# Kernel tuning notes

Measured on AMD Instinct MI355X. Metric: run time of the kernel, lower is better.

Reference implementation:

```python
import jax, jax.numpy as jnp
import numpy as np

DIM = 256
HID = DIM * 16

def setup_inputs() -> dict:
    key = jax.random.key(0)
    ks = jax.random.split(key, 6)
    B, L = 4, 2048
    x = jax.random.normal(ks[0], (B, L, DIM), dtype=jnp.float32)
    # nn.Linear(dim, hidden): weight [H, D], bias [H]
    WB = jax.random.normal(ks[1], (HID, DIM), dtype=jnp.float32) / np.sqrt(DIM)
    bB = jax.random.normal(ks[2], (HID,), dtype=jnp.float32) * 0.01
    # nn.Linear(hidden, dim): weight [D, H], bias [D]
    WC = jax.random.normal(ks[3], (DIM, HID), dtype=jnp.float32) / np.sqrt(HID)
    bC = jax.random.normal(ks[4], (DIM,), dtype=jnp.float32) * 0.01
    A = jax.random.normal(ks[5], (HID,), dtype=jnp.float32)
    return {"x": x, "WB": WB, "bB": bB, "WC": WC, "bC": bC, "A": A}

def reference(x, WB, bB, WC, bC, A):
    # b = B(x): [B, L, H]
    b = jnp.einsum('bld,hd->blh', x, WB) + bB
    a = jax.nn.sigmoid(A)  # [H], time-invariant decay
    # h_t = a * h_{t-1} + b_t  (h_0 from zero state) -> associative scan over L
    a_seq = jnp.broadcast_to(a, b.shape)
    def comb(c1, c2):
        a1, u1 = c1
        a2, u2 = c2
        return (a1 * a2, a2 * u1 + u2)
    _, h = jax.lax.associative_scan(comb, (a_seq, b), axis=1)  # [B, L, H]
    # C(h): [B, L, D]
    return jnp.einsum('blh,dh->bld', h, WC) + bC
```

## Files before the change

kernel.cpp:

```cpp
#include <hip/hip_runtime.h>
#include <hip/hip_bf16.h>

#define DIMSZ 256
#define HID 4096
#define BATCH 4
#define SEQ 2048
#define NCH 64
#define CLEN 32
#define SPLITK2 4
#define KCHUNK (HID / SPLITK2)
#define BM2 32

typedef __bf16 bf16_t;
typedef __bf16 bf16x4 __attribute__((ext_vector_type(4)));
typedef __bf16 bf16x8 __attribute__((ext_vector_type(8)));
typedef float  f32x4  __attribute__((ext_vector_type(4)));

__device__ __forceinline__ float sigmoidf_dev(float x) {
    return 1.0f / (1.0f + __expf(-x));
}

__device__ __forceinline__ bf16x8 cvt8(const float* p) {
    bf16x8 o;
    #pragma unroll
    for (int j = 0; j < 8; j++) o[j] = (bf16_t)p[j];
    return o;
}

__global__ void prep_kernel(const float* __restrict__ x,
                            const float* __restrict__ WB,
                            const float* __restrict__ WC,
                            bf16_t* __restrict__ xt,
                            bf16_t* __restrict__ WBt,
                            bf16_t* __restrict__ Wt) {
    int i = blockIdx.x * blockDim.x + threadIdx.x;
    if (i < 262144) {
        int lane = i & 63, m16 = (i >> 6) & 511, ks = i >> 15;
        int row = m16 * 16 + (lane & 15);
        int k   = ks * 32 + (lane >> 4) * 8;
        *(bf16x8*)&xt[(size_t)i * 8] = cvt8(&x[(size_t)row * DIMSZ + k]);
    } else if (i < 393216) {
        int j = i - 262144;
        int lane = j & 63, n16 = (j >> 6) & 255, ks = j >> 14;
        int row = n16 * 16 + (lane & 15);
        int k   = ks * 32 + (lane >> 4) * 8;
        *(bf16x8*)&WBt[(size_t)j * 8] = cvt8(&WB[(size_t)row * DIMSZ + k]);
    } else {
        int j = i - 393216;
        int lane = j & 63, g = (j >> 6) & 15, ks = j >> 10;
        int row = g * 16 + (lane & 15);
        int k   = ks * 32 + (lane >> 4) * 8;
        *(bf16x8*)&Wt[(size_t)j * 8] = cvt8(&WC[(size_t)row * HID + k]);
    }
}

__global__ __launch_bounds__(256)
void gemm1_fused(const bf16_t* __restrict__ xt, const bf16_t* __restrict__ WBt,
                 const float* __restrict__ bias, const float* __restrict__ Adecay,
                 bf16_t* __restrict__ Cg, float* __restrict__ totals)
{
    constexpr int LDT = 136;
    __shared__ bf16_t tile[128 * LDT];

    const int tid = threadIdx.x, wave = tid >> 6, lane = tid & 63;
    const int wm = wave >> 1, wn = wave & 1, q = lane >> 4, r16 = lane & 15;
    const int mBase = blockIdx.x * 128, nBase = blockIdx.y * 128;
    const int m16Base = blockIdx.x * 8 + wm * 4;
    const int n16Base = blockIdx.y * 8 + wn * 4;
    const int batch = mBase >> 11, tIn = mBase & 2047;
    const int cg0 = tIn >> 5;

    f32x4 acc[4][4] = {};

    #pragma unroll 2
    for (int ks = 0; ks < 8; ks++) {
        bf16x8 af[4], bfr[4];
        #pragma unroll
        for (int mt = 0; mt < 4; mt++)
            af[mt] = *(const bf16x8*)&xt[(((size_t)ks * 512 + m16Base + mt) * 64 + lane) * 8];
        #pragma unroll
        for (int nt = 0; nt < 4; nt++)
            bfr[nt] = *(const bf16x8*)&WBt[(((size_t)ks * 256 + n16Base + nt) * 64 + lane) * 8];
        #pragma unroll
        for (int mt = 0; mt < 4; mt++)
            #pragma unroll
            for (int nt = 0; nt < 4; nt++)
                acc[mt][nt] = __builtin_amdgcn_mfma_f32_16x16x32_bf16(
                    af[mt], bfr[nt], acc[mt][nt], 0, 0, 0);
    }

    #pragma unroll
    for (int nt = 0; nt < 4; nt++) {
        const int chl = wn * 64 + nt * 16 + r16;
        const float bv = bias[nBase + chl];
        #pragma unroll
        for (int mt = 0; mt < 4; mt++) {
            const int t0 = wm * 64 + mt * 16 + q * 4;
            bf16x4 pk;
            #pragma unroll
            for (int rg = 0; rg < 4; rg++)
                pk[rg] = (bf16_t)(acc[mt][nt][rg] + bv);
            *(bf16x4*)&tile[chl * LDT + t0] = pk;
        }
    }
    __syncthreads();

    #pragma unroll
    for (int p = 0; p < 8; p++) {
        const int cc = p >> 1;
        const int tt = (p & 1) * 256 + tid;
        const int ch = tt >> 2, oo = tt & 3;
        *(bf16x8*)&Cg[((size_t)(batch * NCH + cg0 + cc) * HID + nBase + ch) * 32 + oo * 8] =
            *(const bf16x8*)&tile[ch * LDT + cc * 32 + oo * 8];
    }

    #pragma unroll
    for (int t = 0; t < 2; t++) {
        const int task = tid + t * 256;
        const int ch = task & 127, ck = task >> 7;
        const float a = sigmoidf_dev(Adecay[nBase + ch]);
        float tot = 0.f;
        #pragma unroll
        for (int o = 0; o < 4; o++) {
            bf16x8 v8 = *(const bf16x8*)&tile[ch * LDT + ck * CLEN + o * 8];
            #pragma unroll
            for (int j = 0; j < 8; j++)
                tot = a * tot + (float)v8[j];
        }
        totals[(size_t)(batch * NCH + cg0 + ck) * HID + nBase + ch] = tot;
    }
}

__global__ void scan_carries_kernel(const float* __restrict__ totals,
                                    const float* __restrict__ Adecay,
                                    float* __restrict__ carries)
{
    int gid = blockIdx.x * 64 + threadIdx.x;
    int ch    = gid & (HID - 1);
    int batch = gid >> 12;
    float a = sigmoidf_dev(Adecay[ch]);
    float aC = a;
    #pragma unroll
    for (int i = 0; i < 5; i++) aC *= aC;

    float v[NCH];
    #pragma unroll
    for (int c = 0; c < NCH; c++)
        v[c] = totals[(size_t)(batch * NCH + c) * HID + ch];

    float carry = 0.f;
    #pragma unroll
    for (int c = 0; c < NCH; c++) {
        carries[(size_t)(batch * NCH + c) * HID + ch] = carry;
        carry = aC * carry + v[c];
    }
}

#define SCAN_SLAB(REG, S)                                                     \
    do {                                                                      \
        const float a = sigmoidf_dev(aD[S]);                                  \
        float st = sd[S];                                                     \
        bf16_t* hw = &hs[(S) & 1][(tid >> 5) * CKSTRIDE];                     \
        const int cho = (tid >> 3) & 3, chi = tid & 7;                        \
        _Pragma("unroll")                                                     \
        for (int o = 0; o < 4; o++) {                                         \
            _Pragma("unroll")                                                 \
            for (int j = 0; j < 8; j++) {                                     \
                const int t = o * 8 + j;                                      \
                st = a * st + (float)REG[o][j];                               \
                hw[t * 32 + ((cho ^ ((t >> 2) & 3)) << 3) + chi] = (bf16_t)st;\
            }                                                                 \
        }                                                                     \
    } while (0)

__global__ __launch_bounds__(256, 4)
void gemm2_fused(const bf16_t* __restrict__ bv, const bf16_t* __restrict__ Wt,
                 const float* __restrict__ Adecay, const float* __restrict__ carries,
                 bf16_t* __restrict__ P)
{
    constexpr int CKSTRIDE = CLEN * 32 + 32;
    __shared__ bf16_t hs[2][8 * CKSTRIDE];

    const int tid = threadIdx.x, wave = tid >> 6, lane = tid & 63;
    const int q = lane >> 4, r16 = lane & 15;
    const int mBase = blockIdx.x * BM2;
    const int kBase = blockIdx.y * KCHUNK;
    const int batch = mBase >> 11, tIn = mBase & 2047;
    const int chunk = tIn >> 5;

    const bf16_t* bvt = bv + ((size_t)(batch * NCH + chunk) * HID + kBase + tid) * 32;

    bf16x8 rA[4], rB[4];
    #pragma unroll
    for (int o = 0; o < 4; o++)
        rA[o] = *(const bf16x8*)&bvt[o * 8];

    float aD[4], sd[4];
    #pragma unroll
    for (int s = 0; s < 4; s++) {
        const int c = kBase + s * 256 + tid;
        aD[s] = Adecay[c];
        sd[s] = carries[(size_t)(batch * NCH + chunk) * HID + c];
    }

    f32x4 acc[2][4] = {};

    auto mfma_phase = [&](const bf16_t* hb, int s) {
        const int ksBase = (kBase >> 5) + s * 8;
        #pragma unroll 2
        for (int cki = 0; cki < 8; cki++) {
            bf16x8 af[2], bfr[4];
            #pragma unroll
            for (int nt = 0; nt < 4; nt++)
                bfr[nt] = *(const bf16x8*)&Wt[
                    (((size_t)(ksBase + cki) * 16 + wave * 4 + nt) * 64 + lane) * 8];
            #pragma unroll
            for (int mt = 0; mt < 2; mt++)
                af[mt] = *(const bf16x8*)&hb[cki * CKSTRIDE + (mt * 16 + r16) * 32
                                             + ((q ^ (r16 >> 2)) << 3)];
            #pragma unroll
            for (int mt = 0; mt < 2; mt++)
                #pragma unroll
                for (int nt = 0; nt < 4; nt++)
                    acc[mt][nt] = __builtin_amdgcn_mfma_f32_16x16x32_bf16(
                        af[mt], bfr[nt], acc[mt][nt], 0, 0, 0);
        }
    };

    SCAN_SLAB(rA, 0);
    #pragma unroll
    for (int o = 0; o < 4; o++)
        rB[o] = *(const bf16x8*)&bvt[1 * 8192 + o * 8];
    __syncthreads();

    #pragma unroll
    for (int o = 0; o < 4; o++)
        rA[o] = *(const bf16x8*)&bvt[2 * 8192 + o * 8];
    SCAN_SLAB(rB, 1);
    mfma_phase(&hs[0][0], 0);
    __syncthreads();

    #pragma unroll
    for (int o = 0; o < 4; o++)
        rB[o] = *(const bf16x8*)&bvt[3 * 8192 + o * 8];
    SCAN_SLAB(rA, 2);
    mfma_phase(&hs[1][0], 1);
    __syncthreads();

    SCAN_SLAB(rB, 3);
    mfma_phase(&hs[0][0], 2);
    __syncthreads();

    mfma_phase(&hs[1][0], 3);
    #pragma unroll
    for (int nt = 0; nt < 4; nt++) {
        const int col = wave * 64 + nt * 16 + r16;
        #pragma unroll
        for (int mt = 0; mt < 2; mt++)
            #pragma unroll
            for (int rg = 0; rg < 4; rg++)
                hs[0][(mt * 16 + q * 4 + rg) * 264 + col] = (bf16_t)acc[mt][nt][rg];
    }
    __syncthreads();

    bf16_t* Pb = P + (size_t)blockIdx.y * (BATCH * SEQ) * DIMSZ;
    #pragma unroll
    for (int p = 0; p < 4; p++) {
        int task = p * 256 + tid;
        int r = task >> 5, g8 = (task & 31) << 3;
        *(bf16x8*)&Pb[(size_t)(mBase + r) * DIMSZ + g8] =
            *(const bf16x8*)&hs[0][r * 264 + g8];
    }
}

__global__ void reduce_out_kernel(const bf16_t* __restrict__ P,
                                  const float* __restrict__ bias,
                                  float* __restrict__ out, int nTask) {
    int i = blockIdx.x * blockDim.x + threadIdx.x;
    if (i >= nTask) return;
    int n8 = (i & 31) << 3;
    size_t off = (size_t)i * 8;
    float v[8];
    #pragma unroll
    for (int j = 0; j < 8; j++) v[j] = bias[n8 + j];
    #pragma unroll
    for (int sp = 0; sp < SPLITK2; sp++) {
        bf16x8 p = *(const bf16x8*)&P[(size_t)sp * (BATCH * SEQ) * DIMSZ + off];
        #pragma unroll
        for (int j = 0; j < 8; j++) v[j] += (float)p[j];
    }
    float4* o4 = (float4*)&out[off];
    o4[0] = make_float4(v[0], v[1], v[2], v[3]);
    o4[1] = make_float4(v[4], v[5], v[6], v[7]);
}

extern "C" void kernel_launch(void* const* d_in, const int* in_sizes, int n_in,
                              void* d_out, int out_size, void* d_ws, size_t ws_size,
                              hipStream_t stream)
{
    const float* x  = (const float*)d_in[0];
    const float* WB = (const float*)d_in[1];
    const float* bB = (const float*)d_in[2];
    const float* WC = (const float*)d_in[3];
    const float* bC = (const float*)d_in[4];
    const float* A  = (const float*)d_in[5];

    char* ws = (char*)d_ws;
    size_t off = 0;
    bf16_t* xt   = (bf16_t*)(ws + off); off += (size_t)BATCH * SEQ * DIMSZ * 2;
    bf16_t* WBt  = (bf16_t*)(ws + off); off += (size_t)HID * DIMSZ * 2;
    bf16_t* Wt   = (bf16_t*)(ws + off); off += (size_t)DIMSZ * HID * 2;
    bf16_t* bbuf = (bf16_t*)(ws + off); off += (size_t)BATCH * SEQ * HID * 2;
    bf16_t* partials = (bf16_t*)(ws + off); off += (size_t)SPLITK2 * BATCH * SEQ * DIMSZ * 2;
    float* totals   = (float*)(ws + off); off += (size_t)BATCH * NCH * HID * 4;
    float* carries  = (float*)(ws + off); off += (size_t)BATCH * NCH * HID * 4;

    const int M = BATCH * SEQ;

    prep_kernel<<<2048, 256, 0, stream>>>(x, WB, WC, xt, WBt, Wt);

    dim3 g1(M / 128, HID / 128);
    gemm1_fused<<<g1, 256, 0, stream>>>(xt, WBt, bB, A, bbuf, totals);

    scan_carries_kernel<<<256, 64, 0, stream>>>(totals, A, carries);

    dim3 g2(M / BM2, SPLITK2);
    gemm2_fused<<<g2, 256, 0, stream>>>(bbuf, Wt, A, carries, partials);

    int nTask = M * DIMSZ / 8;
    reduce_out_kernel<<<(nTask + 255) / 256, 256, 0, stream>>>(
        partials, bC, (float*)d_out, nTask);
}
```

Measured before the change: 141.1 us.

## Process two time chunks per block in fused scan-GEMM2 to reuse weight loads

Each gemm2_fused block now covers 64 rows (two 32-step chunks) rather than 32. It scans both chunks together into a doubled shared buffer and feeds both into the MFMA loop with a shared set of Wt fragments. This halves the global Wt traffic per output row and halves the grid size. In exchange it doubles register and LDS use and lowers launch bounds occupancy from 4 to 2 blocks per CU.

```diff
diff --git a/kernel.cpp b/kernel.cpp
--- a/kernel.cpp
+++ b/kernel.cpp
@@ -9,7 +9,7 @@
 #define CLEN 32
 #define SPLITK2 4
 #define KCHUNK (HID / SPLITK2)
-#define BM2 32
+#define BM2 64
 
 typedef __bf16 bf16_t;
 typedef __bf16 bf16x4 __attribute__((ext_vector_type(4)));
@@ -156,121 +156,140 @@
     }
 }
 
-#define SCAN_SLAB(REG, S)                                                     \
-    do {                                                                      \
-        const float a = sigmoidf_dev(aD[S]);                                  \
-        float st = sd[S];                                                     \
-        bf16_t* hw = &hs[(S) & 1][(tid >> 5) * CKSTRIDE];                     \
-        const int cho = (tid >> 3) & 3, chi = tid & 7;                        \
-        _Pragma("unroll")                                                     \
-        for (int o = 0; o < 4; o++) {                                         \
-            _Pragma("unroll")                                                 \
-            for (int j = 0; j < 8; j++) {                                     \
-                const int t = o * 8 + j;                                      \
-                st = a * st + (float)REG[o][j];                               \
-                hw[t * 32 + ((cho ^ ((t >> 2) & 3)) << 3) + chi] = (bf16_t)st;\
-            }                                                                 \
-        }                                                                     \
-    } while (0)
-
-__global__ __launch_bounds__(256, 4)
+__global__ __launch_bounds__(256, 2)
 void gemm2_fused(const bf16_t* __restrict__ bv, const bf16_t* __restrict__ Wt,
                  const float* __restrict__ Adecay, const float* __restrict__ carries,
                  bf16_t* __restrict__ P)
 {
     constexpr int CKSTRIDE = CLEN * 32 + 32;
-    __shared__ bf16_t hs[2][8 * CKSTRIDE];
+    constexpr int CHOFF = 8 * CKSTRIDE;
+    __shared__ bf16_t hs[2][2 * CHOFF];
 
     const int tid = threadIdx.x, wave = tid >> 6, lane = tid & 63;
     const int q = lane >> 4, r16 = lane & 15;
     const int mBase = blockIdx.x * BM2;
     const int kBase = blockIdx.y * KCHUNK;
     const int batch = mBase >> 11, tIn = mBase & 2047;
-    const int chunk = tIn >> 5;
-
-    const bf16_t* bvt = bv + ((size_t)(batch * NCH + chunk) * HID + kBase + tid) * 32;
-
-    bf16x8 rA[4], rB[4];
-    #pragma unroll
-    for (int o = 0; o < 4; o++)
-        rA[o] = *(const bf16x8*)&bvt[o * 8];
-
-    float aD[4], sd[4];
+    const int chunk0 = tIn >> 5;
+
+    const size_t base0 = ((size_t)(batch * NCH + chunk0) * HID + kBase + tid) * 32;
+    const size_t base1 = base0 + (size_t)HID * 32;
+
+    bf16x8 rA[8], rB[8];
+
+    #define LOAD_SLAB(R, S)                                                   \
+        do {                                                                  \
+            _Pragma("unroll")                                                 \
+            for (int o = 0; o < 4; o++) {                                     \
+                R[o]     = *(const bf16x8*)&bv[base0 + (S) * 8192 + o * 8];   \
+                R[4 + o] = *(const bf16x8*)&bv[base1 + (S) * 8192 + o * 8];   \
+            }                                                                 \
+        } while (0)
+
+    LOAD_SLAB(rA, 0);
+
+    float aD[4], sd0[4], sd1[4];
     #pragma unroll
     for (int s = 0; s < 4; s++) {
         const int c = kBase + s * 256 + tid;
-        aD[s] = Adecay[c];
-        sd[s] = carries[(size_t)(batch * NCH + chunk) * HID + c];
-    }
-
-    f32x4 acc[2][4] = {};
+        aD[s]  = Adecay[c];
+        sd0[s] = carries[(size_t)(batch * NCH + chunk0) * HID + c];
+        sd1[s] = carries[(size_t)(batch * NCH + chunk0 + 1) * HID + c];
+    }
+
+    LOAD_SLAB(rB, 1);
+
+    f32x4 acc[2][2][4] = {};
+
+    #define SCAN_SLAB(R, S, PG)                                               \
+        do {                                                                  \
+            const float a = sigmoidf_dev(aD[S]);                              \
+            float st0 = sd0[S], st1 = sd1[S];                                 \
+            bf16_t* hw0 = &hs[PG][(tid >> 5) * CKSTRIDE];                     \
+            bf16_t* hw1 = hw0 + CHOFF;                                        \
+            const int cho = (tid >> 3) & 3, chi = tid & 7;                    \
+            _Pragma("unroll")                                                 \
+            for (int o = 0; o < 4; o++) {                                     \
+                _Pragma("unroll")                                             \
+                for (int j = 0; j < 8; j++) {                                 \
+                    const int t = o * 8 + j;                                  \
+                    const int sw = t * 32 + ((cho ^ ((t >> 2) & 3)) << 3) + chi; \
+                    st0 = a * st0 + (float)R[o][j];                           \
+                    hw0[sw] = (bf16_t)st0;                                    \
+                    st1 = a * st1 + (float)R[4 + o][j];                       \
+                    hw1[sw] = (bf16_t)st1;                                    \
+                }                                                             \
+            }                                                                 \
+        } while (0)
 
     auto mfma_phase = [&](const bf16_t* hb, int s) {
         const int ksBase = (kBase >> 5) + s * 8;
         #pragma unroll 2
         for (int cki = 0; cki < 8; cki++) {
-            bf16x8 af[2], bfr[4];
+            bf16x8 af[2][2], bfr[4];
             #pragma unroll
             for (int nt = 0; nt < 4; nt++)
                 bfr[nt] = *(const bf16x8*)&Wt[
                     (((size_t)(ksBase + cki) * 16 + wave * 4 + nt) * 64 + lane) * 8];
             #pragma unroll
-            for (int mt = 0; mt < 2; mt++)
-                af[mt] = *(const bf16x8*)&hb[cki * CKSTRIDE + (mt * 16 + r16) * 32
-                                             + ((q ^ (r16 >> 2)) << 3)];
+            for (int c = 0; c < 2; c++)
+                #pragma unroll
+                for (int mt = 0; mt < 2; mt++)
+                    af[c][mt] = *(const bf16x8*)&hb[c * CHOFF + cki * CKSTRIDE
+                                 + (mt * 16 + r16) * 32 + ((q ^ (r16 >> 2)) << 3)];
+            #pragma unroll
+            for (int c = 0; c < 2; c++)
+                #pragma unroll
+                for (int mt = 0; mt < 2; mt++)
+                    #pragma unroll
+                    for (int nt = 0; nt < 4; nt++)
+                        acc[c][mt][nt] = __builtin_amdgcn_mfma_f32_16x16x32_bf16(
+                            af[c][mt], bfr[nt], acc[c][mt][nt], 0, 0, 0);
+        }
+    };
+
+    SCAN_SLAB(rA, 0, 0);
+    __syncthreads();
+
+    LOAD_SLAB(rA, 2);
+    SCAN_SLAB(rB, 1, 1);
+    mfma_phase(&hs[0][0], 0);
+    __syncthreads();
+
+    LOAD_SLAB(rB, 3);
+    SCAN_SLAB(rA, 2, 0);
+    mfma_phase(&hs[1][0], 1);
+    __syncthreads();
+
+    SCAN_SLAB(rB, 3, 1);
+    mfma_phase(&hs[0][0], 2);
+    __syncthreads();
+
+    mfma_phase(&hs[1][0], 3);
+    #pragma unroll
+    for (int nt = 0; nt < 4; nt++) {
+        const int col = wave * 64 + nt * 16 + r16;
+        #pragma unroll
+        for (int c = 0; c < 2; c++)
             #pragma unroll
             for (int mt = 0; mt < 2; mt++)
                 #pragma unroll
-                for (int nt = 0; nt < 4; nt++)
-                    acc[mt][nt] = __builtin_amdgcn_mfma_f32_16x16x32_bf16(
-                        af[mt], bfr[nt], acc[mt][nt], 0, 0, 0);
-        }
-    };
-
-    SCAN_SLAB(rA, 0);
-    #pragma unroll
-    for (int o = 0; o < 4; o++)
-        rB[o] = *(const bf16x8*)&bvt[1 * 8192 + o * 8];
-    __syncthreads();
-
-    #pragma unroll
-    for (int o = 0; o < 4; o++)
-        rA[o] = *(const bf16x8*)&bvt[2 * 8192 + o * 8];
-    SCAN_SLAB(rB, 1);
-    mfma_phase(&hs[0][0], 0);
-    __syncthreads();
-
-    #pragma unroll
-    for (int o = 0; o < 4; o++)
-        rB[o] = *(const bf16x8*)&bvt[3 * 8192 + o * 8];
-    SCAN_SLAB(rA, 2);
-    mfma_phase(&hs[1][0], 1);
-    __syncthreads();
-
-    SCAN_SLAB(rB, 3);
-    mfma_phase(&hs[0][0], 2);
-    __syncthreads();
-
-    mfma_phase(&hs[1][0], 3);
-    #pragma unroll
-    for (int nt = 0; nt < 4; nt++) {
-        const int col = wave * 64 + nt * 16 + r16;
-        #pragma unroll
-        for (int mt = 0; mt < 2; mt++)
-            #pragma unroll
-            for (int rg = 0; rg < 4; rg++)
-                hs[0][(mt * 16 + q * 4 + rg) * 264 + col] = (bf16_t)acc[mt][nt][rg];
+                for (int rg = 0; rg < 4; rg++)
+                    hs[0][(c * 32 + mt * 16 + q * 4 + rg) * 264 + col] =
+                        (bf16_t)acc[c][mt][nt][rg];
     }
     __syncthreads();
 
     bf16_t* Pb = P + (size_t)blockIdx.y * (BATCH * SEQ) * DIMSZ;
     #pragma unroll
-    for (int p = 0; p < 4; p++) {
-        int task = p * 256 + tid;
-        int r = task >> 5, g8 = (task & 31) << 3;
+    for (int p = 0; p < 8; p++) {
+        const int task = p * 256 + tid;
+        const int r = task >> 5, g8 = (task & 31) << 3;
         *(bf16x8*)&Pb[(size_t)(mBase + r) * DIMSZ + g8] =
             *(const bf16x8*)&hs[0][r * 264 + g8];
     }
+    #undef LOAD_SLAB
+    #undef SCAN_SLAB
 }
 
 __global__ void reduce_out_kernel(const bf16_t* __restrict__ P,
```

Result: no change. 139.6 us (-1.0%).
